# Kernel tuning notes

Hardware: AMD Instinct MI355X
Metric: run time of the kernel (lower is better)

The kernel has to match this reference:

```python
import math
import jax, jax.numpy as jnp
import numpy as np

TEMPERATURE = 1.0
N_SAMPLES = 7
B, D = 2048, 512

def _l2_normalize(x, eps=1e-12):
    return x / jnp.maximum(jnp.linalg.norm(x, axis=-1, keepdims=True), eps)

def setup_inputs() -> dict:
    key = jax.random.key(0)
    ks = jax.random.split(key, 7)
    return {
        "query_mean": jax.random.normal(ks[0], (B, D), jnp.float32),
        "query_logsigma": jax.random.normal(ks[1], (B, D), jnp.float32),
        "query_z": jax.random.normal(ks[2], (B,), jnp.float32),
        "target_mean": jax.random.normal(ks[3], (B, D), jnp.float32),
        "target_logsigma": jax.random.normal(ks[4], (B, D), jnp.float32),
        "target_z": jax.random.normal(ks[5], (B,), jnp.float32),
        "eps": jax.random.normal(ks[6], (B, N_SAMPLES, D), jnp.float32),
    }

def reference(query_mean, query_logsigma, query_z, target_mean, target_logsigma, target_z, eps):
    qm = _l2_normalize(query_mean)                       # [B, D]
    tm = _l2_normalize(target_mean)                      # [B, D]
    # sample_gaussian_tensors: mu + eps * exp(logsigma), 7 samples -> [B, 7, D]
    samples = tm[:, None, :] + eps * jnp.exp(target_logsigma)[:, None, :]
    inv_sigmas = jnp.exp(-query_logsigma)                # [B, D] per-query precisions
    # weighted squared distance via the GEMM trick:
    # sum_d (t - q)^2 * w = sum_d t^2 w - 2 sum_d t q w + sum_d q^2 w
    t_term = jnp.einsum('qd,tsd->qts', inv_sigmas, samples * samples)   # [Bq, Bt, 7]
    x_term = jnp.einsum('qd,tsd->qts', qm * inv_sigmas, samples)        # [Bq, Bt, 7]
    q_term = jnp.sum(qm * qm * inv_sigmas, axis=-1)                     # [Bq]
    sqdist = t_term - 2.0 * x_term + q_term[:, None, None]
    loc = -0.5 * jnp.mean(sqdist, axis=-1)                              # [Bq, Bt]
    d = qm.shape[-1]
    norm_constant = (-d / 2.0) * jnp.log(jnp.float32(2.0 * math.pi)) \
                    - 0.5 * jnp.sum(query_logsigma, axis=-1)            # [Bq]
    # NOTE: torch broadcasting aligns the [B] vectors to the LAST (target) axis
    scores = query_z + norm_constant + loc                              # [Bq, Bt]
    scores = scores - jnp.max(scores, axis=0, keepdims=True)
    logits = scores / TEMPERATURE
    logp = jax.nn.log_softmax(logits, axis=-1)
    idx = jnp.arange(scores.shape[0])
    loss = -jnp.mean(logp[idx, idx])                                    # reduction='mean'
    return loss

if __name__ == "__main__":
    print(reference(**setup_inputs()))
```

## Files before the change

kernel.cpp:

```cpp
#include <hip/hip_runtime.h>
#include <math.h>

#define BB 2048
#define DD 512
#define NS 7
#define KK 1024
#define BM 128
#define BN 64
#define BK 64
#define NT (KK / BK)

typedef __attribute__((ext_vector_type(8))) short short8;
typedef __attribute__((ext_vector_type(4))) float floatx4;
typedef long long i64;

typedef const __attribute__((address_space(1))) void gv_t;
typedef __attribute__((address_space(3))) void lv_t;
__device__ __forceinline__ void gl2lds16(const void* g, void* l) {
  __builtin_amdgcn_global_load_lds((gv_t*)g, (lv_t*)l, 16, 0, 0);
}

__device__ __forceinline__ unsigned short f2bf(float f) {
  unsigned int u = __float_as_uint(f);
  u += 0x7FFFu + ((u >> 16) & 1u);
  return (unsigned short)(u >> 16);
}
__device__ __forceinline__ float bf2f(unsigned short u) {
  return __uint_as_float(((unsigned)u) << 16);
}

__device__ __forceinline__ unsigned fkey(float f) {
  unsigned u = __float_as_uint(f);
  return (u & 0x80000000u) ? ~u : (u | 0x80000000u);
}
__device__ __forceinline__ float funkey(unsigned k) {
  unsigned u = (k & 0x80000000u) ? (k ^ 0x80000000u) : ~k;
  return __uint_as_float(u);
}

__device__ __forceinline__ uint2 pack8_fp8(const float* v) {
  int lo = 0, hi = 0;
  lo = __builtin_amdgcn_cvt_pk_fp8_f32(v[0], v[1], lo, false);
  lo = __builtin_amdgcn_cvt_pk_fp8_f32(v[2], v[3], lo, true);
  hi = __builtin_amdgcn_cvt_pk_fp8_f32(v[4], v[5], hi, false);
  hi = __builtin_amdgcn_cvt_pk_fp8_f32(v[6], v[7], hi, true);
  uint2 r; r.x = (unsigned)lo; r.y = (unsigned)hi; return r;
}


__device__ __forceinline__ float wsum(float v) {
#pragma unroll
  for (int off = 32; off > 0; off >>= 1) v += __shfl_xor(v, off, 64);
  return v;
}
__device__ __forceinline__ float wmax(float v) {
#pragma unroll
  for (int off = 32; off > 0; off >>= 1) v = fmaxf(v, __shfl_xor(v, off, 64));
  return v;
}
__device__ __forceinline__ float block_reduce_sum256(float v, float* sbuf) {
  v = wsum(v);
  if ((threadIdx.x & 63) == 0) sbuf[threadIdx.x >> 6] = v;
  __syncthreads();
  float r = sbuf[0] + sbuf[1] + sbuf[2] + sbuf[3];
  __syncthreads();
  return r;
}

__global__ __launch_bounds__(256) void prep(
    const float* __restrict__ qmean, const float* __restrict__ qls,
    const float* __restrict__ tmean, const float* __restrict__ tls,
    const float* __restrict__ eps,
    unsigned char* __restrict__ Acat, unsigned char* __restrict__ Bcat,
    float* __restrict__ qterm, unsigned* __restrict__ Mkey) {
  const int w = threadIdx.x >> 6, lane = threadIdx.x & 63;
  const int r = blockIdx.x * 4 + w;
  const int grp = (lane >> 3) * 64;
  const int physoff = (((((lane & 7) >> 1) ^ r) & 3) << 4) |
                      ((((lane & 7) ^ (r >> 2)) & 1) << 3);
  if (r < BB) {
    const int q = r;
    const float4* xm = (const float4*)(qmean + (size_t)q * DD);
    const float4* xl = (const float4*)(qls + (size_t)q * DD);
    float4 a0 = xm[2 * lane], a1 = xm[2 * lane + 1];
    float4 l0 = xl[2 * lane], l1 = xl[2 * lane + 1];
    float x[8] = {a0.x, a0.y, a0.z, a0.w, a1.x, a1.y, a1.z, a1.w};
    float l[8] = {l0.x, l0.y, l0.z, l0.w, l1.x, l1.y, l1.z, l1.w};
    float ss = 0.f;
#pragma unroll
    for (int e = 0; e < 8; ++e) ss += x[e] * x[e];
    ss = wsum(ss);
    float inv = 1.0f / fmaxf(sqrtf(ss), 1e-12f);
    float W[8], M2[8], qt = 0.f;
#pragma unroll
    for (int e = 0; e < 8; ++e) {
      W[e] = expf(-l[e]);
      float n = x[e] * inv;
      M2[e] = -2.0f * n * W[e];
      qt += n * n * W[e];
    }
    qt = wsum(qt);
    if (lane == 0) qterm[q] = qt;
    unsigned char* arow = Acat + (size_t)q * KK;
    *(uint2*)(arow + grp + physoff)       = pack8_fp8(W);
    *(uint2*)(arow + 512 + grp + physoff) = pack8_fp8(M2);
  } else {
    const int t = r - BB;
    if (lane == 0) Mkey[t] = 0u;
    const float4* xm = (const float4*)(tmean + (size_t)t * DD);
    const float4* xl = (const float4*)(tls + (size_t)t * DD);
    float4 a0 = xm[2 * lane], a1 = xm[2 * lane + 1];
    float4 l0 = xl[2 * lane], l1 = xl[2 * lane + 1];
    float x[8] = {a0.x, a0.y, a0.z, a0.w, a1.x, a1.y, a1.z, a1.w};
    float l[8] = {l0.x, l0.y, l0.z, l0.w, l1.x, l1.y, l1.z, l1.w};
    float ss = 0.f;
#pragma unroll
    for (int e = 0; e < 8; ++e) ss += x[e] * x[e];
    ss = wsum(ss);
    float inv = 1.0f / fmaxf(sqrtf(ss), 1e-12f);
    float se[8], sq[8];
#pragma unroll
    for (int e = 0; e < 8; ++e) { se[e] = 0.f; sq[e] = 0.f; }
    const float4* ep = (const float4*)(eps + (size_t)t * NS * DD);
#pragma unroll
    for (int s = 0; s < NS; ++s) {
      float4 e0 = ep[s * (DD / 4) + 2 * lane];
      float4 e1 = ep[s * (DD / 4) + 2 * lane + 1];
      float ev[8] = {e0.x, e0.y, e0.z, e0.w, e1.x, e1.y, e1.z, e1.w};
#pragma unroll
      for (int e = 0; e < 8; ++e) { se[e] += ev[e]; sq[e] += ev[e] * ev[e]; }
    }
    const float i7 = 1.0f / 7.0f;
    float S2[8], S1[8];
#pragma unroll
    for (int e = 0; e < 8; ++e) {
      float tm = x[e] * inv;
      float sg = expf(l[e]);
      float m1 = sg * se[e] * i7;
      S1[e] = tm + m1;
      S2[e] = (tm * tm + 2.0f * tm * m1 + sg * sg * sq[e] * i7) * 0.00390625f;
    }
    unsigned char* brow = Bcat + (size_t)t * KK;
    *(uint2*)(brow + grp + physoff)       = pack8_fp8(S2);
    *(uint2*)(brow + 512 + grp + physoff) = pack8_fp8(S1);
  }
}

__global__ __launch_bounds__(256) void gemm_loc(
    const unsigned char* __restrict__ Acat,
    const unsigned char* __restrict__ Bcat,
    const float* __restrict__ qterm,
    unsigned short* __restrict__ loc, unsigned* __restrict__ Mkey) {
  __shared__ __align__(16) char As[3][BM * BK];
  __shared__ __align__(16) char Bs[3][BN * BK];
  const int tid = threadIdx.x, lane = tid & 63, wid = tid >> 6;
  const int lin = blockIdx.y * (BB / BN) + blockIdx.x;
  const int xcd = lin & 7, j = lin >> 3;
  const int tr = ((xcd >> 2) << 3) + (j >> 3);
  const int tc = ((xcd & 3) << 3) + (j & 7);
  const int brow = tr * BM, bcol = tc * BN;
  const int wr = wid >> 1, wc = wid & 1;
  const int fr = lane & 15, kg = lane >> 4;

  floatx4 acc[2][4][2];
#pragma unroll
  for (int h = 0; h < 2; ++h)
#pragma unroll
    for (int m = 0; m < 4; ++m)
#pragma unroll
      for (int n = 0; n < 2; ++n) acc[h][m][n] = (floatx4){0.f, 0.f, 0.f, 0.f};

  const unsigned char* gA0 = Acat + (size_t)(brow + (tid >> 2)) * KK + (tid & 3) * 16;
  const unsigned char* gA1 = gA0 + (size_t)64 * KK;
  const unsigned char* gB0 = Bcat + (size_t)(bcol + (tid >> 2)) * KK + (tid & 3) * 16;

#define STAGE(buf, kc)                                      \
  {                                                         \
    gl2lds16(gA0 + (kc), &As[buf][tid * 16]);               \
    gl2lds16(gA1 + (kc), &As[buf][4096 + tid * 16]);        \
    gl2lds16(gB0 + (kc), &Bs[buf][tid * 16]);               \
  }

  STAGE(0, 0)
  STAGE(1, BK)

#pragma unroll
  for (int kt = 0; kt < NT; ++kt) {
    if (kt < NT - 1) asm volatile("s_waitcnt vmcnt(3)" ::: "memory");
    else             asm volatile("s_waitcnt vmcnt(0)" ::: "memory");
    __builtin_amdgcn_s_barrier();
    if (kt + 2 < NT) { STAGE((kt + 2) % 3, (kt + 2) * BK) }
    const char* a  = As[kt % 3];
    const char* bp = Bs[kt % 3];
#pragma unroll
    for (int kh = 0; kh < 2; ++kh) {
      const int co = ((((kh * 2 + (kg >> 1)) ^ fr) & 3) << 4) |
                     (((kg ^ (fr >> 2)) & 1) << 3);
      i64 af[4], bf[2];
#pragma unroll
      for (int m = 0; m < 4; ++m)
        af[m] = *(const i64*)(a + (wr * 64 + m * 16 + fr) * BK + co);
#pragma unroll
      for (int n = 0; n < 2; ++n)
        bf[n] = *(const i64*)(bp + (wc * 32 + n * 16 + fr) * BK + co);
      __builtin_amdgcn_s_setprio(1);
#pragma unroll
      for (int m = 0; m < 4; ++m)
#pragma unroll
        for (int n = 0; n < 2; ++n)
          acc[kt >> 3][m][n] = __builtin_amdgcn_mfma_f32_16x16x32_fp8_fp8(
              af[m], bf[n], acc[kt >> 3][m][n], 0, 0, 0);
      __builtin_amdgcn_s_setprio(0);
    }
  }
#undef STAGE

#pragma unroll
  for (int n = 0; n < 2; ++n) {
    const int col = bcol + wc * 32 + n * 16 + fr;
    float cm = -3.402823466e38f;
#pragma unroll
    for (int m = 0; m < 4; ++m) {
      const int row = brow + wr * 64 + m * 16 + kg * 4;
#pragma unroll
      for (int r4 = 0; r4 < 4; ++r4) {
        float v = -0.5f * (256.0f * acc[0][m][n][r4] + acc[1][m][n][r4] +
                           qterm[row + r4]);
        loc[(size_t)(row + r4) * BB + col] = f2bf(v);
        cm = fmaxf(cm, v);
      }
    }
    cm = fmaxf(cm, __shfl_xor(cm, 16, 64));
    cm = fmaxf(cm, __shfl_xor(cm, 32, 64));
    if (kg == 0) atomicMax(&Mkey[col], fkey(cm));
  }
}

__global__ __launch_bounds__(256) void row_lse(
    const unsigned short* __restrict__ loc, const unsigned* __restrict__ Mkey,
    float* __restrict__ rowval) {
  const int w = threadIdx.x >> 6, lane = threadIdx.x & 63;
  const int q = blockIdx.x * 4 + w;
  const short8* lp = (const short8*)(loc + (size_t)q * BB);
  const uint4* kp = (const uint4*)Mkey;
  float xs[4][8];
  float m = -3.402823466e38f, dv = 0.f;
#pragma unroll
  for (int c = 0; c < 4; ++c) {
    short8 v = lp[c * 64 + lane];
    uint4 k0 = kp[(c * 64 + lane) * 2];
    uint4 k1 = kp[(c * 64 + lane) * 2 + 1];
    unsigned ks[8] = {k0.x, k0.y, k0.z, k0.w, k1.x, k1.y, k1.z, k1.w};
#pragma unroll
    for (int e = 0; e < 8; ++e) {
      float x = bf2f((unsigned short)v[e]) - funkey(ks[e]);
      xs[c][e] = x;
      m = fmaxf(m, x);
      if (c * 512 + lane * 8 + e == q) dv = x;
    }
  }
  m = wmax(m);
  float s = 0.f;
#pragma unroll
  for (int c = 0; c < 4; ++c)
#pragma unroll
    for (int e = 0; e < 8; ++e) s += expf(xs[c][e] - m);
  s = wsum(s);
  float d = __shfl(dv, (q >> 3) & 63, 64);
  if (lane == 0) rowval[q] = d - (m + logf(s));
}

__global__ __launch_bounds__(256) void final_loss(
    const float* __restrict__ rowval, float* __restrict__ out) {
  __shared__ float sbuf[4];
  const int tid = threadIdx.x;
  float s = 0.f;
#pragma unroll
  for (int i = 0; i < 8; ++i) s += rowval[tid + i * 256];
  s = block_reduce_sum256(s, sbuf);
  if (tid == 0) out[0] = -s * (1.0f / (float)BB);
}

extern "C" void kernel_launch(void* const* d_in, const int* in_sizes, int n_in,
                              void* d_out, int out_size, void* d_ws, size_t ws_size,
                              hipStream_t stream) {
  const float* qmean = (const float*)d_in[0];
  const float* qls   = (const float*)d_in[1];
  const float* tmean = (const float*)d_in[3];
  const float* tls   = (const float*)d_in[4];
  const float* eps   = (const float*)d_in[6];

  char* ws = (char*)d_ws;
  unsigned char* Acat  = (unsigned char*)(ws + 0);
  unsigned char* Bcat  = (unsigned char*)(ws + (2u << 20));
  float* qterm         = (float*)(ws + (4u << 20));
  unsigned* Mkey       = (unsigned*)(ws + (4u << 20) + 8192);
  float* rowval        = (float*)(ws + (4u << 20) + 16384);
  unsigned short* loc  = (unsigned short*)(ws + (4u << 20) + 65536);

  prep<<<1024, 256, 0, stream>>>(qmean, qls, tmean, tls, eps,
                                 Acat, Bcat, qterm, Mkey);
  gemm_loc<<<dim3(BB / BN, BB / BM), 256, 0, stream>>>(Acat, Bcat, qterm, loc, Mkey);
  row_lse<<<512, 256, 0, stream>>>(loc, Mkey, rowval);
  final_loss<<<1, 256, 0, stream>>>(rowval, (float*)d_out);
}
```

Before: 34.93 us.

## Fuse GEMM, row log-sum-exp and final loss into one kernel with grid barriers

Merges the GEMM, the row log-sum-exp and the final reduction into one persistent kernel of 512 blocks. Atomic-counter grid barriers separate the column-max, row-max and row-sum phases, and the scores stay in registers instead of being written to and reread from a bf16 score matrix. Row sums are accumulated as fixed-point 64-bit integer atomics. This removes the 8 MB score-matrix round trip and two kernel launches, but it relies on all 512 blocks being co-resident and adds spin waits plus many atomics.

```diff
diff --git a/kernel.cpp b/kernel.cpp
--- a/kernel.cpp
+++ b/kernel.cpp
@@ -10,23 +10,14 @@
 #define BK 64
 #define NT (KK / BK)
 
-typedef __attribute__((ext_vector_type(8))) short short8;
 typedef __attribute__((ext_vector_type(4))) float floatx4;
 typedef long long i64;
+typedef unsigned long long u64;
 
 typedef const __attribute__((address_space(1))) void gv_t;
 typedef __attribute__((address_space(3))) void lv_t;
 __device__ __forceinline__ void gl2lds16(const void* g, void* l) {
   __builtin_amdgcn_global_load_lds((gv_t*)g, (lv_t*)l, 16, 0, 0);
-}
-
-__device__ __forceinline__ unsigned short f2bf(float f) {
-  unsigned int u = __float_as_uint(f);
-  u += 0x7FFFu + ((u >> 16) & 1u);
-  return (unsigned short)(u >> 16);
-}
-__device__ __forceinline__ float bf2f(unsigned short u) {
-  return __uint_as_float(((unsigned)u) << 16);
 }
 
 __device__ __forceinline__ unsigned fkey(float f) {
@@ -47,24 +38,10 @@
   uint2 r; r.x = (unsigned)lo; r.y = (unsigned)hi; return r;
 }
 
-
 __device__ __forceinline__ float wsum(float v) {
 #pragma unroll
   for (int off = 32; off > 0; off >>= 1) v += __shfl_xor(v, off, 64);
   return v;
-}
-__device__ __forceinline__ float wmax(float v) {
-#pragma unroll
-  for (int off = 32; off > 0; off >>= 1) v = fmaxf(v, __shfl_xor(v, off, 64));
-  return v;
-}
-__device__ __forceinline__ float block_reduce_sum256(float v, float* sbuf) {
-  v = wsum(v);
-  if ((threadIdx.x & 63) == 0) sbuf[threadIdx.x >> 6] = v;
-  __syncthreads();
-  float r = sbuf[0] + sbuf[1] + sbuf[2] + sbuf[3];
-  __syncthreads();
-  return r;
 }
 
 __global__ __launch_bounds__(256) void prep(
@@ -72,7 +49,9 @@
     const float* __restrict__ tmean, const float* __restrict__ tls,
     const float* __restrict__ eps,
     unsigned char* __restrict__ Acat, unsigned char* __restrict__ Bcat,
-    float* __restrict__ qterm, unsigned* __restrict__ Mkey) {
+    float* __restrict__ qterm, unsigned* __restrict__ Mkey,
+    unsigned* __restrict__ rmax, u64* __restrict__ rowsum,
+    unsigned* __restrict__ cnt) {
   const int w = threadIdx.x >> 6, lane = threadIdx.x & 63;
   const int r = blockIdx.x * 4 + w;
   const int grp = (lane >> 3) * 64;
@@ -80,6 +59,10 @@
                       ((((lane & 7) ^ (r >> 2)) & 1) << 3);
   if (r < BB) {
     const int q = r;
+    if (q == 0) {
+      cnt[lane] = 0u;
+      cnt[64 + lane] = 0u;
+    }
     const float4* xm = (const float4*)(qmean + (size_t)q * DD);
     const float4* xl = (const float4*)(qls + (size_t)q * DD);
     float4 a0 = xm[2 * lane], a1 = xm[2 * lane + 1];
@@ -106,7 +89,11 @@
     *(uint2*)(arow + 512 + grp + physoff) = pack8_fp8(M2);
   } else {
     const int t = r - BB;
-    if (lane == 0) Mkey[t] = 0u;
+    if (lane == 0) {
+      Mkey[t] = 0u;
+      rmax[t] = 0u;
+      rowsum[t] = 0ull;
+    }
     const float4* xm = (const float4*)(tmean + (size_t)t * DD);
     const float4* xl = (const float4*)(tls + (size_t)t * DD);
     float4 a0 = xm[2 * lane], a1 = xm[2 * lane + 1];
@@ -146,16 +133,21 @@
   }
 }
 
-__global__ __launch_bounds__(256) void gemm_loc(
+__global__ __launch_bounds__(256) void fused_loss(
     const unsigned char* __restrict__ Acat,
     const unsigned char* __restrict__ Bcat,
     const float* __restrict__ qterm,
-    unsigned short* __restrict__ loc, unsigned* __restrict__ Mkey) {
+    unsigned* __restrict__ Mkey, unsigned* __restrict__ rmax,
+    unsigned* __restrict__ diagv, u64* __restrict__ rowsum,
+    unsigned* __restrict__ cnt, float* __restrict__ out) {
   __shared__ __align__(16) char As[3][BM * BK];
   __shared__ __align__(16) char Bs[3][BN * BK];
+  __shared__ unsigned mk[64];
+  __shared__ float rmx[128];
+  __shared__ float sb[4];
   const int tid = threadIdx.x, lane = tid & 63, wid = tid >> 6;
-  const int lin = blockIdx.y * (BB / BN) + blockIdx.x;
-  const int xcd = lin & 7, j = lin >> 3;
+  const int bid = blockIdx.x;
+  const int xcd = bid & 7, j = bid >> 3;
   const int tr = ((xcd >> 2) << 3) + (j >> 3);
   const int tc = ((xcd & 3) << 3) + (j & 7);
   const int brow = tr * BM, bcol = tc * BN;
@@ -215,70 +207,126 @@
   }
 #undef STAGE
 
+  floatx4 cv[4][2];
+#pragma unroll
+  for (int m = 0; m < 4; ++m) {
+    const int row = brow + wr * 64 + m * 16 + kg * 4;
+#pragma unroll
+    for (int r4 = 0; r4 < 4; ++r4) {
+      float qt = qterm[row + r4];
+#pragma unroll
+      for (int n = 0; n < 2; ++n)
+        cv[m][n][r4] = -0.5f * (256.0f * acc[0][m][n][r4] + acc[1][m][n][r4] + qt);
+    }
+  }
 #pragma unroll
   for (int n = 0; n < 2; ++n) {
-    const int col = bcol + wc * 32 + n * 16 + fr;
     float cm = -3.402823466e38f;
 #pragma unroll
-    for (int m = 0; m < 4; ++m) {
-      const int row = brow + wr * 64 + m * 16 + kg * 4;
-#pragma unroll
-      for (int r4 = 0; r4 < 4; ++r4) {
-        float v = -0.5f * (256.0f * acc[0][m][n][r4] + acc[1][m][n][r4] +
-                           qterm[row + r4]);
-        loc[(size_t)(row + r4) * BB + col] = f2bf(v);
-        cm = fmaxf(cm, v);
-      }
-    }
+    for (int m = 0; m < 4; ++m)
+#pragma unroll
+      for (int r4 = 0; r4 < 4; ++r4) cm = fmaxf(cm, cv[m][n][r4]);
     cm = fmaxf(cm, __shfl_xor(cm, 16, 64));
     cm = fmaxf(cm, __shfl_xor(cm, 32, 64));
-    if (kg == 0) atomicMax(&Mkey[col], fkey(cm));
-  }
-}
-
-__global__ __launch_bounds__(256) void row_lse(
-    const unsigned short* __restrict__ loc, const unsigned* __restrict__ Mkey,
-    float* __restrict__ rowval) {
-  const int w = threadIdx.x >> 6, lane = threadIdx.x & 63;
-  const int q = blockIdx.x * 4 + w;
-  const short8* lp = (const short8*)(loc + (size_t)q * BB);
-  const uint4* kp = (const uint4*)Mkey;
-  float xs[4][8];
-  float m = -3.402823466e38f, dv = 0.f;
-#pragma unroll
-  for (int c = 0; c < 4; ++c) {
-    short8 v = lp[c * 64 + lane];
-    uint4 k0 = kp[(c * 64 + lane) * 2];
-    uint4 k1 = kp[(c * 64 + lane) * 2 + 1];
-    unsigned ks[8] = {k0.x, k0.y, k0.z, k0.w, k1.x, k1.y, k1.z, k1.w};
-#pragma unroll
-    for (int e = 0; e < 8; ++e) {
-      float x = bf2f((unsigned short)v[e]) - funkey(ks[e]);
-      xs[c][e] = x;
-      m = fmaxf(m, x);
-      if (c * 512 + lane * 8 + e == q) dv = x;
-    }
-  }
-  m = wmax(m);
+    if (kg == 0) atomicMax(&Mkey[bcol + wc * 32 + n * 16 + fr], fkey(cm));
+  }
+
+  __syncthreads();
+  if (tid == 0) {
+    unsigned v = atomicAdd(&cnt[bid & 31], 1u);
+    if (v == 15u) atomicAdd(&cnt[32], 1u);
+    for (int it = 0; it < (1 << 20); ++it) {
+      if (__hip_atomic_load(&cnt[32], __ATOMIC_RELAXED,
+                            __HIP_MEMORY_SCOPE_AGENT) >= 32u) break;
+      __builtin_amdgcn_s_sleep(4);
+    }
+  }
+  __syncthreads();
+
+  if (tid < 64) mk[tid] = atomicMax(&Mkey[bcol + tid], 0u);
+  __syncthreads();
+  const float Mn0 = funkey(mk[wc * 32 + fr]);
+  const float Mn1 = funkey(mk[wc * 32 + 16 + fr]);
+  const int col0 = bcol + wc * 32 + fr, col1 = col0 + 16;
+
+#pragma unroll
+  for (int m = 0; m < 4; ++m) {
+#pragma unroll
+    for (int r4 = 0; r4 < 4; ++r4) {
+      const int row = brow + wr * 64 + m * 16 + kg * 4 + r4;
+      float x0 = cv[m][0][r4] - Mn0;
+      float x1 = cv[m][1][r4] - Mn1;
+      cv[m][0][r4] = x0; cv[m][1][r4] = x1;
+      if (row == col0) atomicExch(&diagv[row], __float_as_uint(x0));
+      if (row == col1) atomicExch(&diagv[row], __float_as_uint(x1));
+      float xm = fmaxf(x0, x1);
+      xm = fmaxf(xm, __shfl_xor(xm, 1, 64));
+      xm = fmaxf(xm, __shfl_xor(xm, 2, 64));
+      xm = fmaxf(xm, __shfl_xor(xm, 4, 64));
+      xm = fmaxf(xm, __shfl_xor(xm, 8, 64));
+      if (fr == 0) atomicMax(&rmax[row], fkey(xm));
+    }
+  }
+
+  __syncthreads();
+  if (tid == 0) {
+    unsigned v = atomicAdd(&cnt[33 + (bid & 31)], 1u);
+    if (v == 15u) atomicAdd(&cnt[65], 1u);
+    for (int it = 0; it < (1 << 20); ++it) {
+      if (__hip_atomic_load(&cnt[65], __ATOMIC_RELAXED,
+                            __HIP_MEMORY_SCOPE_AGENT) >= 32u) break;
+      __builtin_amdgcn_s_sleep(4);
+    }
+  }
+  __syncthreads();
+
+  if (tid < 128) rmx[tid] = funkey(atomicMax(&rmax[brow + tid], 0u));
+  __syncthreads();
+
+#pragma unroll
+  for (int m = 0; m < 4; ++m) {
+#pragma unroll
+    for (int r4 = 0; r4 < 4; ++r4) {
+      const int rloc = wr * 64 + m * 16 + kg * 4 + r4;
+      const float rm = rmx[rloc];
+      float e = expf(cv[m][0][r4] - rm) + expf(cv[m][1][r4] - rm);
+      e += __shfl_xor(e, 1, 64);
+      e += __shfl_xor(e, 2, 64);
+      e += __shfl_xor(e, 4, 64);
+      e += __shfl_xor(e, 8, 64);
+      if (fr == 0)
+        atomicAdd(&rowsum[brow + rloc], (u64)(e * 1.7592186044416e13f));
+    }
+  }
+
+  __syncthreads();
+  if (tid == 0) {
+    unsigned v = atomicAdd(&cnt[66 + (bid & 31)], 1u);
+    if (v == 15u) atomicAdd(&cnt[98], 1u);
+    if (bid == 0) {
+      for (int it = 0; it < (1 << 20); ++it) {
+        if (__hip_atomic_load(&cnt[98], __ATOMIC_RELAXED,
+                              __HIP_MEMORY_SCOPE_AGENT) >= 32u) break;
+        __builtin_amdgcn_s_sleep(4);
+      }
+    }
+  }
+  __syncthreads();
+  if (bid != 0) return;
+
   float s = 0.f;
 #pragma unroll
-  for (int c = 0; c < 4; ++c)
-#pragma unroll
-    for (int e = 0; e < 8; ++e) s += expf(xs[c][e] - m);
+  for (int i = 0; i < 8; ++i) {
+    int q = tid + i * 256;
+    float dg = __uint_as_float(diagv[q]);
+    float rm = funkey(rmax[q]);
+    float rs = (float)rowsum[q] * 5.6843418860808015e-14f;
+    s += dg - rm - logf(rs);
+  }
   s = wsum(s);
-  float d = __shfl(dv, (q >> 3) & 63, 64);
-  if (lane == 0) rowval[q] = d - (m + logf(s));
-}
-
-__global__ __launch_bounds__(256) void final_loss(
-    const float* __restrict__ rowval, float* __restrict__ out) {
-  __shared__ float sbuf[4];
-  const int tid = threadIdx.x;
-  float s = 0.f;
-#pragma unroll
-  for (int i = 0; i < 8; ++i) s += rowval[tid + i * 256];
-  s = block_reduce_sum256(s, sbuf);
-  if (tid == 0) out[0] = -s * (1.0f / (float)BB);
+  if (lane == 0) sb[wid] = s;
+  __syncthreads();
+  if (tid == 0) out[0] = -(sb[0] + sb[1] + sb[2] + sb[3]) * (1.0f / (float)BB);
 }
 
 extern "C" void kernel_launch(void* const* d_in, const int* in_sizes, int n_in,
@@ -291,16 +339,17 @@
   const float* eps   = (const float*)d_in[6];
 
   char* ws = (char*)d_ws;
-  unsigned char* Acat  = (unsigned char*)(ws + 0);
-  unsigned char* Bcat  = (unsigned char*)(ws + (2u << 20));
-  float* qterm         = (float*)(ws + (4u << 20));
-  unsigned* Mkey       = (unsigned*)(ws + (4u << 20) + 8192);
-  float* rowval        = (float*)(ws + (4u << 20) + 16384);
-  unsigned short* loc  = (unsigned short*)(ws + (4u << 20) + 65536);
+  unsigned char* Acat = (unsigned char*)(ws);
+  unsigned char* Bcat = (unsigned char*)(ws + (2u << 20));
+  float* qterm  = (float*)(ws + (4u << 20));
+  unsigned* Mkey = (unsigned*)(ws + (4u << 20) + 8192);
+  unsigned* rmax = (unsigned*)(ws + (4u << 20) + 16384);
+  unsigned* diagv = (unsigned*)(ws + (4u << 20) + 24576);
+  u64* rowsum = (u64*)(ws + (4u << 20) + 32768);
+  unsigned* cnt = (unsigned*)(ws + (4u << 20) + 49152);
 
   prep<<<1024, 256, 0, stream>>>(qmean, qls, tmean, tls, eps,
-                                 Acat, Bcat, qterm, Mkey);
-  gemm_loc<<<dim3(BB / BN, BB / BM), 256, 0, stream>>>(Acat, Bcat, qterm, loc, Mkey);
-  row_lse<<<512, 256, 0, stream>>>(loc, Mkey, rowval);
-  final_loss<<<1, 256, 0, stream>>>(rowval, (float*)d_out);
-}
+                                 Acat, Bcat, qterm, Mkey, rmax, rowsum, cnt);
+  fused_loss<<<512, 256, 0, stream>>>(Acat, Bcat, qterm, Mkey, rmax, diagv,
+                                      rowsum, cnt, (float*)d_out);
+}
```

Measured after the change: 53.71 us. 1.54x slower.

## Double GEMM K-tile to 128 with new swizzle and fuse final loss into row_lse

Applied to the files above, without the earlier changes.

The GEMM K-tile grows from 64 to 128, so there are half as many barrier and stage iterations. The prep layout swizzle and the LDS read offsets are rewritten to match the wider 128-byte rows. The final_loss launch is removed: the last row_lse block, found through a two-level atomic counter, does the global sum. This saves one kernel launch and some barrier overhead, at the cost of more LDS (three buffers of 24KB) and possibly lower occupancy.

```diff
diff --git a/kernel.cpp b/kernel.cpp
--- a/kernel.cpp
+++ b/kernel.cpp
@@ -7,12 +7,13 @@
 #define KK 1024
 #define BM 128
 #define BN 64
-#define BK 64
+#define BK 128
 #define NT (KK / BK)
 
 typedef __attribute__((ext_vector_type(8))) short short8;
 typedef __attribute__((ext_vector_type(4))) float floatx4;
 typedef long long i64;
+typedef unsigned long long u64;
 
 typedef const __attribute__((address_space(1))) void gv_t;
 typedef __attribute__((address_space(3))) void lv_t;
@@ -58,28 +59,21 @@
   for (int off = 32; off > 0; off >>= 1) v = fmaxf(v, __shfl_xor(v, off, 64));
   return v;
 }
-__device__ __forceinline__ float block_reduce_sum256(float v, float* sbuf) {
-  v = wsum(v);
-  if ((threadIdx.x & 63) == 0) sbuf[threadIdx.x >> 6] = v;
-  __syncthreads();
-  float r = sbuf[0] + sbuf[1] + sbuf[2] + sbuf[3];
-  __syncthreads();
-  return r;
-}
 
 __global__ __launch_bounds__(256) void prep(
     const float* __restrict__ qmean, const float* __restrict__ qls,
     const float* __restrict__ tmean, const float* __restrict__ tls,
     const float* __restrict__ eps,
     unsigned char* __restrict__ Acat, unsigned char* __restrict__ Bcat,
-    float* __restrict__ qterm, unsigned* __restrict__ Mkey) {
+    float* __restrict__ qterm, unsigned* __restrict__ Mkey,
+    unsigned* __restrict__ cnt) {
   const int w = threadIdx.x >> 6, lane = threadIdx.x & 63;
   const int r = blockIdx.x * 4 + w;
-  const int grp = (lane >> 3) * 64;
-  const int physoff = (((((lane & 7) >> 1) ^ r) & 3) << 4) |
-                      ((((lane & 7) ^ (r >> 2)) & 1) << 3);
+  const int grp = (lane >> 4) * 128;
+  const int physoff = ((lane & 15) ^ (r & 15)) << 3;
   if (r < BB) {
     const int q = r;
+    if (q == 0) cnt[lane] = 0u;
     const float4* xm = (const float4*)(qmean + (size_t)q * DD);
     const float4* xl = (const float4*)(qls + (size_t)q * DD);
     float4 a0 = xm[2 * lane], a1 = xm[2 * lane + 1];
@@ -170,15 +164,18 @@
 #pragma unroll
       for (int n = 0; n < 2; ++n) acc[h][m][n] = (floatx4){0.f, 0.f, 0.f, 0.f};
 
-  const unsigned char* gA0 = Acat + (size_t)(brow + (tid >> 2)) * KK + (tid & 3) * 16;
-  const unsigned char* gA1 = gA0 + (size_t)64 * KK;
-  const unsigned char* gB0 = Bcat + (size_t)(bcol + (tid >> 2)) * KK + (tid & 3) * 16;
-
-#define STAGE(buf, kc)                                      \
-  {                                                         \
-    gl2lds16(gA0 + (kc), &As[buf][tid * 16]);               \
-    gl2lds16(gA1 + (kc), &As[buf][4096 + tid * 16]);        \
-    gl2lds16(gB0 + (kc), &Bs[buf][tid * 16]);               \
+  const unsigned char* gA0 = Acat + (size_t)(brow + (tid >> 3)) * KK + (tid & 7) * 16;
+  const unsigned char* gB0 = Bcat + (size_t)(bcol + (tid >> 3)) * KK + (tid & 7) * 16;
+  const int ldst = (tid >> 3) * 128 + (tid & 7) * 16;
+
+#define STAGE(buf, kc)                                                   \
+  {                                                                      \
+    _Pragma("unroll")                                                    \
+    for (int j2 = 0; j2 < 4; ++j2)                                       \
+      gl2lds16(gA0 + (size_t)j2 * 32 * KK + (kc), &As[buf][ldst + j2 * 4096]); \
+    _Pragma("unroll")                                                    \
+    for (int j2 = 0; j2 < 2; ++j2)                                       \
+      gl2lds16(gB0 + (size_t)j2 * 32 * KK + (kc), &Bs[buf][ldst + j2 * 4096]); \
   }
 
   STAGE(0, 0)
@@ -186,16 +183,15 @@
 
 #pragma unroll
   for (int kt = 0; kt < NT; ++kt) {
-    if (kt < NT - 1) asm volatile("s_waitcnt vmcnt(3)" ::: "memory");
+    if (kt < NT - 1) asm volatile("s_waitcnt vmcnt(6)" ::: "memory");
     else             asm volatile("s_waitcnt vmcnt(0)" ::: "memory");
     __builtin_amdgcn_s_barrier();
     if (kt + 2 < NT) { STAGE((kt + 2) % 3, (kt + 2) * BK) }
     const char* a  = As[kt % 3];
     const char* bp = Bs[kt % 3];
 #pragma unroll
-    for (int kh = 0; kh < 2; ++kh) {
-      const int co = ((((kh * 2 + (kg >> 1)) ^ fr) & 3) << 4) |
-                     (((kg ^ (fr >> 2)) & 1) << 3);
+    for (int kh = 0; kh < 4; ++kh) {
+      const int co = (((kh * 4 + kg) ^ fr) & 15) << 3;
       i64 af[4], bf[2];
 #pragma unroll
       for (int m = 0; m < 4; ++m)
@@ -208,8 +204,8 @@
       for (int m = 0; m < 4; ++m)
 #pragma unroll
         for (int n = 0; n < 2; ++n)
-          acc[kt >> 3][m][n] = __builtin_amdgcn_mfma_f32_16x16x32_fp8_fp8(
-              af[m], bf[n], acc[kt >> 3][m][n], 0, 0, 0);
+          acc[kt >> 2][m][n] = __builtin_amdgcn_mfma_f32_16x16x32_fp8_fp8(
+              af[m], bf[n], acc[kt >> 2][m][n], 0, 0, 0);
       __builtin_amdgcn_s_setprio(0);
     }
   }
@@ -238,8 +234,11 @@
 
 __global__ __launch_bounds__(256) void row_lse(
     const unsigned short* __restrict__ loc, const unsigned* __restrict__ Mkey,
-    float* __restrict__ rowval) {
-  const int w = threadIdx.x >> 6, lane = threadIdx.x & 63;
+    unsigned* __restrict__ rowval, unsigned* __restrict__ cnt,
+    float* __restrict__ out) {
+  __shared__ int lastflag;
+  __shared__ float sb[4];
+  const int w = threadIdx.x >> 6, lane = threadIdx.x & 63, tid = threadIdx.x;
   const int q = blockIdx.x * 4 + w;
   const short8* lp = (const short8*)(loc + (size_t)q * BB);
   const uint4* kp = (const uint4*)Mkey;
@@ -267,18 +266,35 @@
     for (int e = 0; e < 8; ++e) s += expf(xs[c][e] - m);
   s = wsum(s);
   float d = __shfl(dv, (q >> 3) & 63, 64);
-  if (lane == 0) rowval[q] = d - (m + logf(s));
-}
-
-__global__ __launch_bounds__(256) void final_loss(
-    const float* __restrict__ rowval, float* __restrict__ out) {
-  __shared__ float sbuf[4];
-  const int tid = threadIdx.x;
-  float s = 0.f;
-#pragma unroll
-  for (int i = 0; i < 8; ++i) s += rowval[tid + i * 256];
-  s = block_reduce_sum256(s, sbuf);
-  if (tid == 0) out[0] = -s * (1.0f / (float)BB);
+  if (lane == 0)
+    atomicExch(&rowval[q], __float_as_uint(d - (m + logf(s))));
+
+  __syncthreads();
+  if (tid == 0) {
+    __threadfence();
+    int last = 0;
+    unsigned t1 = atomicAdd(&cnt[blockIdx.x & 31], 1u);
+    if (t1 == 15u) {
+      unsigned t2 = atomicAdd(&cnt[32], 1u);
+      last = (t2 == 31u);
+    }
+    lastflag = last;
+  }
+  __syncthreads();
+  if (!lastflag) return;
+  __threadfence();
+
+  float fs = 0.f;
+#pragma unroll
+  for (int i = 0; i < 8; ++i) {
+    unsigned u = __hip_atomic_load(&rowval[tid + i * 256], __ATOMIC_RELAXED,
+                                   __HIP_MEMORY_SCOPE_AGENT);
+    fs += __uint_as_float(u);
+  }
+  fs = wsum(fs);
+  if (lane == 0) sb[w] = fs;
+  __syncthreads();
+  if (tid == 0) out[0] = -(sb[0] + sb[1] + sb[2] + sb[3]) * (1.0f / (float)BB);
 }
 
 extern "C" void kernel_launch(void* const* d_in, const int* in_sizes, int n_in,
@@ -291,16 +307,16 @@
   const float* eps   = (const float*)d_in[6];
 
   char* ws = (char*)d_ws;
-  unsigned char* Acat  = (unsigned char*)(ws + 0);
-  unsigned char* Bcat  = (unsigned char*)(ws + (2u << 20));
-  float* qterm         = (float*)(ws + (4u << 20));
-  unsigned* Mkey       = (unsigned*)(ws + (4u << 20) + 8192);
-  float* rowval        = (float*)(ws + (4u << 20) + 16384);
-  unsigned short* loc  = (unsigned short*)(ws + (4u << 20) + 65536);
+  unsigned char* Acat = (unsigned char*)(ws);
+  unsigned char* Bcat = (unsigned char*)(ws + (2u << 20));
+  float* qterm   = (float*)(ws + (4u << 20));
+  unsigned* Mkey = (unsigned*)(ws + (4u << 20) + 8192);
+  unsigned* rowval = (unsigned*)(ws + (4u << 20) + 16384);
+  unsigned* cnt  = (unsigned*)(ws + (4u << 20) + 24576);
+  unsigned short* loc = (unsigned short*)(ws + (4u << 20) + 65536);
 
   prep<<<1024, 256, 0, stream>>>(qmean, qls, tmean, tls, eps,
-                                 Acat, Bcat, qterm, Mkey);
+                                 Acat, Bcat, qterm, Mkey, cnt);
   gemm_loc<<<dim3(BB / BN, BB / BM), 256, 0, stream>>>(Acat, Bcat, qterm, loc, Mkey);
-  row_lse<<<512, 256, 0, stream>>>(loc, Mkey, rowval);
-  final_loss<<<1, 256, 0, stream>>>(rowval, (float*)d_out);
-}
+  row_lse<<<512, 256, 0, stream>>>(loc, Mkey, rowval, cnt, (float*)d_out);
+}
```

After: 39.59 us. 1.13x slower.
